# Optimization experiments

Hardware: AMD Instinct MI355X
Metric: run time of the kernel (lower is better)

## Reference

```python
import jax, jax.numpy as jnp
import numpy as np

EPS = 1e-5

def _offset_conv(x, w, b):
    # 3x3 conv, padding=1, producing 2*K*K offset channels (standard DeformConv2D v1)
    out = jax.lax.conv_general_dilated(x, w, (1, 1), ((1, 1), (1, 1)),
                                       dimension_numbers=('NCHW', 'OIHW', 'NCHW'))
    return out + b[None, :, None, None]

def _bilinear_gather(x, py, px):
    # x: [B,C,H,W]; py,px: [B,K2,H,W] float sample coords -> [B,C,K2,H,W]
    B, C, H, W = x.shape
    py = jnp.clip(py, 0.0, H - 1.0)
    px = jnp.clip(px, 0.0, W - 1.0)
    y0 = jnp.floor(py)
    x0 = jnp.floor(px)
    wy = py - y0
    wx = px - x0
    y0i = y0.astype(jnp.int32)
    x0i = x0.astype(jnp.int32)
    y1i = jnp.minimum(y0i + 1, H - 1)
    x1i = jnp.minimum(x0i + 1, W - 1)
    xf = x.reshape(B, C, H * W)
    K2, Ho, Wo = py.shape[1], py.shape[2], py.shape[3]
    def gather(yy, xx):
        idx = (yy * W + xx).reshape(B, 1, -1)  # broadcast over C
        return jnp.take_along_axis(xf, idx, axis=2).reshape(B, C, K2, Ho, Wo)
    v00 = gather(y0i, x0i)
    v01 = gather(y0i, x1i)
    v10 = gather(y1i, x0i)
    v11 = gather(y1i, x1i)
    wy = wy[:, None]
    wx = wx[:, None]
    return (v00 * (1 - wy) * (1 - wx) + v01 * (1 - wy) * wx
            + v10 * wy * (1 - wx) + v11 * wy * wx)

def _deform_dw(x, w_off, b_off, w_dw, k):
    # depthwise deformable conv, kernel k, padding k//2 (same spatial size)
    B, C, H, W = x.shape
    K2 = k * k
    off = _offset_conv(x, w_off, b_off)      # [B, 2*K2, H, W]
    dy, dx = off[:, :K2], off[:, K2:]
    r = (k - 1) // 2
    pn = jnp.arange(-r, r + 1, dtype=x.dtype)
    pn_y = jnp.repeat(pn, k)[None, :, None, None]  # [1,K2,1,1]
    pn_x = jnp.tile(pn, k)[None, :, None, None]
    gy = jnp.arange(H, dtype=x.dtype)[None, None, :, None]
    gx = jnp.arange(W, dtype=x.dtype)[None, None, None, :]
    py = gy + pn_y + dy
    px = gx + pn_x + dx
    samp = _bilinear_gather(x, py, px)        # [B,C,K2,H,W]
    return jnp.einsum('bckhw,ck->bchw', samp, w_dw.reshape(C, K2))

def _bn_relu(x, g, b, m, v):
    inv = g / jnp.sqrt(v + EPS)
    return jax.nn.relu(x * inv[None, :, None, None] + (b - m * inv)[None, :, None, None])

def setup_inputs() -> dict:
    key = jax.random.key(0)
    B, C, H, W, O = 4, 96, 64, 64, 192
    ks = jax.random.split(key, 32)
    d = {'x': jax.random.normal(ks[0], (B, C, H, W), jnp.float32)}
    i = 1
    for k in (3, 5, 7):
        K2 = k * k
        d[f'w_off{k}'] = 0.01 * jax.random.normal(ks[i], (2 * K2, C, 3, 3), jnp.float32); i += 1
        d[f'b_off{k}'] = jnp.zeros((2 * K2,), jnp.float32)
        d[f'w_dw{k}'] = jax.random.normal(ks[i], (C, k, k), jnp.float32) / k; i += 1
        d[f'g{k}'] = jnp.ones((C,), jnp.float32)
        d[f'be{k}'] = jnp.zeros((C,), jnp.float32)
        d[f'm{k}'] = 0.1 * jax.random.normal(ks[i], (C,), jnp.float32); i += 1
        d[f'v{k}'] = jax.random.uniform(ks[i], (C,), jnp.float32, 0.5, 1.5); i += 1
    d['w_pw'] = jax.random.normal(ks[i], (O, 3 * C), jnp.float32) / np.sqrt(3 * C).astype(np.float32); i += 1
    d['gp'] = jnp.ones((O,), jnp.float32)
    d['bp'] = jnp.zeros((O,), jnp.float32)
    d['mp'] = 0.1 * jax.random.normal(ks[i], (O,), jnp.float32); i += 1
    d['vp'] = jax.random.uniform(ks[i], (O,), jnp.float32, 0.5, 1.5)
    return d

def reference(x, w_off3, b_off3, w_dw3, g3, be3, m3, v3,
              w_off5, b_off5, w_dw5, g5, be5, m5, v5,
              w_off7, b_off7, w_dw7, g7, be7, m7, v7,
              w_pw, gp, bp, mp, vp):
    x1 = _bn_relu(_deform_dw(x, w_off3, b_off3, w_dw3, 3), g3, be3, m3, v3)
    x2 = _bn_relu(_deform_dw(x, w_off5, b_off5, w_dw5, 5), g5, be5, m5, v5)
    x3 = _bn_relu(_deform_dw(x, w_off7, b_off7, w_dw7, 7), g7, be7, m7, v7)
    xc = jnp.concatenate([x1, x2, x3], axis=1)  # [B, 3C, H, W]
    out = jnp.einsum('bchw,oc->bohw', xc, w_pw)  # 1x1 conv
    return _bn_relu(out, gp, bp, mp, vp)
```

## Files before the change

### kernel.cpp

```cpp
#include <hip/hip_runtime.h>
#include <math.h>

typedef unsigned short u16;
typedef short s16x8 __attribute__((ext_vector_type(8)));
typedef float f32x4 __attribute__((ext_vector_type(4)));

#define HWp 4096
#define Cc 96
#define Bb 4
#define Oo 192
#define C3 288

#define OFF_OFF   0
#define OFF_WDWT  3145728
#define OFF_BCAT  3159840
#define OFF_SBR   3160032
#define OFF_HBR   3160320
#define OFF_SPW   3160608
#define OFF_HPW   3160800
#define FP32_END  3160992
#define BF_XTPAD  0
#define BF_WOF    1672704
#define BF_WPW    1838592
#define BF_YT     1893888

__device__ __forceinline__ u16 f2bf(float f) {
    union { float f; unsigned u; } t; t.f = f;
    unsigned u = t.u;
    return (u16)((u + 0x7fffu + ((u >> 16) & 1u)) >> 16);
}
__device__ __forceinline__ float bflo(unsigned u) { return __uint_as_float(u << 16); }
__device__ __forceinline__ float bfhi(unsigned u) { return __uint_as_float(u & 0xffff0000u); }

__global__ __launch_bounds__(256) void prep_kernel(
    const float* __restrict__ w3, const float* __restrict__ b3, const float* __restrict__ dw3,
    const float* __restrict__ g3, const float* __restrict__ be3, const float* __restrict__ m3, const float* __restrict__ v3,
    const float* __restrict__ w5, const float* __restrict__ b5, const float* __restrict__ dw5,
    const float* __restrict__ g5, const float* __restrict__ be5, const float* __restrict__ m5, const float* __restrict__ v5,
    const float* __restrict__ w7, const float* __restrict__ b7, const float* __restrict__ dw7,
    const float* __restrict__ g7, const float* __restrict__ be7, const float* __restrict__ m7, const float* __restrict__ v7,
    const float* __restrict__ wpw,
    const float* __restrict__ gp, const float* __restrict__ bp, const float* __restrict__ mp, const float* __restrict__ vp,
    float* __restrict__ ws)
{
    u16* bf = (u16*)(ws + FP32_END);
    int i = blockIdx.x * 256 + threadIdx.x;
    if (i < 165888) {
        int f = i / 13824, r = i % 13824;
        int s = r >> 9, l = r & 511;
        int lane = l >> 3, j = l & 7;
        int o = f * 16 + (lane & 15);
        int k = s * 32 + (lane >> 4) * 8 + j;
        int tap = k / 96, c = k % 96;
        float v = 0.f;
        if (o < 18)       v = w3[o * 864 + c * 9 + tap];
        else if (o < 68)  v = w5[(o - 18) * 864 + c * 9 + tap];
        else if (o < 166) v = w7[(o - 68) * 864 + c * 9 + tap];
        bf[BF_WOF + i] = f2bf(v);
        return;
    }
    int j = i - 165888;
    if (j < 55296) {
        int f = j / 4608, r = j % 4608;
        int s = r >> 9, l = r & 511;
        int lane = l >> 3, jj = l & 7;
        int o = f * 16 + (lane & 15);
        int k = s * 32 + (lane >> 4) * 8 + jj;
        bf[BF_WPW + j] = f2bf(wpw[o * C3 + k]);
        return;
    }
    j -= 55296;
    if (j < 14112) {
        int ksel = j / 4704, rem = j % 4704;
        int t = rem / 96, c = rem % 96;
        int K2 = (ksel == 0) ? 9 : (ksel == 1) ? 25 : 49;
        const float* dw = (ksel == 0) ? dw3 : (ksel == 1) ? dw5 : dw7;
        ws[OFF_WDWT + j] = (t < K2) ? dw[c * K2 + t] : 0.f;
        return;
    }
    j -= 14112;
    if (j < 192) {
        float v = 0.f;
        if (j < 18)       v = b3[j];
        else if (j < 68)  v = b5[j - 18];
        else if (j < 166) v = b7[j - 68];
        ws[OFF_BCAT + j] = v;
        return;
    }
    j -= 192;
    if (j < C3) {
        int ks = j / Cc, c = j % Cc;
        const float* g = (ks == 0) ? g3 : (ks == 1) ? g5 : g7;
        const float* v = (ks == 0) ? v3 : (ks == 1) ? v5 : v7;
        ws[OFF_SBR + j] = g[c] / sqrtf(v[c] + 1e-5f);
        return;
    }
    j -= C3;
    if (j < C3) {
        int ks = j / Cc, c = j % Cc;
        const float* g = (ks == 0) ? g3 : (ks == 1) ? g5 : g7;
        const float* v = (ks == 0) ? v3 : (ks == 1) ? v5 : v7;
        const float* be = (ks == 0) ? be3 : (ks == 1) ? be5 : be7;
        const float* m = (ks == 0) ? m3 : (ks == 1) ? m5 : m7;
        float inv = g[c] / sqrtf(v[c] + 1e-5f);
        ws[OFF_HBR + j] = be[c] - m[c] * inv;
        return;
    }
    j -= C3;
    if (j < Oo) { ws[OFF_SPW + j] = gp[j] / sqrtf(vp[j] + 1e-5f); return; }
    j -= Oo;
    if (j < Oo) {
        float inv = gp[j] / sqrtf(vp[j] + 1e-5f);
        ws[OFF_HPW + j] = bp[j] - mp[j] * inv;
        return;
    }
    j -= Oo;
    if (j < 24960) {
        int c4 = j % 24, rem = j / 24;
        int cell = rem % 260, bb = rem / 260;
        int row, col;
        if (cell < 66)       { row = 0;  col = cell; }
        else if (cell < 132) { row = 65; col = cell - 66; }
        else if (cell < 196) { row = cell - 132 + 1; col = 0; }
        else                 { row = cell - 196 + 1; col = 65; }
        u16* dst = bf + BF_XTPAD + ((size_t)(bb * 66 + row) * 66 + col) * 96 + c4 * 4;
        *(uint2*)dst = make_uint2(0u, 0u);
        return;
    }
}
#define PREP_N (165888 + 55296 + 14112 + 192 + 288 + 288 + 192 + 192 + 24960)

__global__ __launch_bounds__(256) void xtpad_kernel(
    const float* __restrict__ x, float* __restrict__ ws)
{
    __shared__ u16 sT[64 * 104];
    u16* bfm = (u16*)(ws + FP32_END);
    const int tid = threadIdx.x;
    const int h = blockIdx.x, b = blockIdx.y;
    const float* xb = x + (((size_t)b * Cc) << 12) + (h << 6);
#pragma unroll
    for (int it = 0; it < 24; ++it) {
        int j = tid + it * 256;
        int c = j >> 6, p = j & 63;
        sT[p * 104 + c] = f2bf(xb[((size_t)c << 12) + p]);
    }
    __syncthreads();
    u16* dst = bfm + BF_XTPAD + ((size_t)(b * 66 + h + 1) * 66 + 1) * 96;
#pragma unroll
    for (int it = 0; it < 6; ++it) {
        int j = tid + it * 256;
        int pos = j / 24, c4 = j % 24;
        const u16* s = &sT[pos * 104 + c4 * 4];
        *(uint2*)(dst + pos * 96 + c4 * 4) = make_uint2(
            (unsigned)s[0] | ((unsigned)s[1] << 16),
            (unsigned)s[2] | ((unsigned)s[3] << 16));
    }
}

__global__ __launch_bounds__(512) void offconv_mfma(
    const float* __restrict__ ws, float* __restrict__ off)
{
    __shared__ u16 sX[3 * 66 * 98];
    const u16* bf = (const u16*)(ws + FP32_END);
    const u16* xp = bf + BF_XTPAD;
    const u16* wof = bf + BF_WOF;
    const int tid = threadIdx.x;
    const int lane = tid & 63, wid = tid >> 6;
    const int lane15 = lane & 15, quad = lane >> 4;
    const int h = blockIdx.x;
    const int b = blockIdx.z;
    const int f0 = (wid >> 2) * 6;
    const int pos = (wid & 3) * 16 + lane15;

#pragma unroll
    for (int it = 0; it < 10; ++it) {
        int j = tid + it * 512;
        if (j < 4752) {
            int r = j / (66 * 24);
            int rem = j % (66 * 24);
            int col = rem / 24, c4 = rem % 24;
            uint2 v = *(const uint2*)(xp + ((size_t)((b * 66 + h + r) * 66 + col)) * 96 + c4 * 4);
            *(uint2*)(&sX[(r * 66 + col) * 98 + c4 * 4]) = v;
        }
    }
    __syncthreads();

    f32x4 acc[6];
#pragma unroll
    for (int f = 0; f < 6; ++f) acc[f] = (f32x4){0.f, 0.f, 0.f, 0.f};

#pragma unroll
    for (int tap = 0; tap < 9; ++tap) {
        const int ky = tap / 3, kx = tap % 3;
        const u16* brow = &sX[(ky * 66 + kx + pos) * 98 + quad * 8];
#pragma unroll
        for (int cc = 0; cc < 3; ++cc) {
            s16x8 bb = *(const s16x8*)(brow + cc * 32);
            const int s = tap * 3 + cc;
#pragma unroll
            for (int f = 0; f < 6; ++f) {
                s16x8 a = *(const s16x8*)(wof + ((size_t)((f0 + f) * 27 + s) * 64 + lane) * 8);
                acc[f] = __builtin_amdgcn_mfma_f32_16x16x32_bf16(a, bb, acc[f], 0, 0, 0);
            }
        }
    }

    const float* bcat = ws + OFF_BCAT;
    const int p = (h << 6) + pos;
#pragma unroll
    for (int f = 0; f < 6; ++f) {
        float* dst = off + (((size_t)(b * 192 + (f0 + f) * 16 + quad * 4)) << 12) + p;
#pragma unroll
        for (int r = 0; r < 4; ++r)
            dst[(size_t)r << 12] = acc[f][r] + bcat[(f0 + f) * 16 + quad * 4 + r];
    }
}

template<int K>
__device__ __forceinline__ void samp_v6(
    int ksel, float* __restrict__ sWI,
    const float* __restrict__ ws, u16* __restrict__ yt)
{
    constexpr int K2 = K * K;
    constexpr int R = (K - 1) / 2;
    const int tb = (ksel == 0) ? 0 : ((ksel == 1) ? 18 : 68);

    const int tid = threadIdx.x;
    const int b = blockIdx.z;
    const int p0 = blockIdx.x * 20;

    const float* offb = ws + OFF_OFF + ((size_t)(b * 192 + tb)) * HWp;
    for (int i = tid; i < K2 * 20; i += 256) {
        int t = i / 20, q = i % 20;
        int p = min(p0 + q, 4095);
        int hh = p >> 6, wp = p & 63;
        float dy = offb[(size_t)t * HWp + p];
        float dx = offb[(size_t)(K2 + t) * HWp + p];
        int ky = t / K - R, kx = t % K - R;
        float py = fminf(fmaxf((float)(hh + ky) + dy, 0.f), 63.f);
        float px = fminf(fmaxf((float)(wp + kx) + dx, 0.f), 63.f);
        float fy = floorf(py), fx = floorf(px);
        int y0 = (int)fy, x0 = (int)fx;
        float wy = py - fy, wx = px - fx;
        int y1 = min(y0 + 1, 63), x1 = min(x0 + 1, 63);
        float w11 = wy * wx;
        float w10 = wy - w11;
        float w01 = wx - w11;
        float w00 = 1.f - wy - wx + w11;
        float* dst = &sWI[i * 8];
        dst[0] = w00; dst[1] = w01; dst[2] = w10; dst[3] = w11;
        dst[4] = __int_as_float(((y0 + 1) * 66 + x0 + 1) * 96);
        dst[5] = __int_as_float(((y0 + 1) * 66 + x1 + 1) * 96);
        dst[6] = __int_as_float(((y1 + 1) * 66 + x0 + 1) * 96);
        dst[7] = __int_as_float(((y1 + 1) * 66 + x1 + 1) * 96);
    }
    __syncthreads();

    const int c8 = tid % 12;
    const int q  = tid / 12;
    const int p  = p0 + q;
    if (tid < 240 && p < 4096) {
        const int c = c8 * 8;

        const u16* xc = (const u16*)(ws + FP32_END) + BF_XTPAD + (size_t)b * 66 * 66 * 96 + c;
        const float* wdT = ws + OFF_WDWT + ksel * 4704 + c;

        float acc[8];
#pragma unroll
        for (int k = 0; k < 8; ++k) acc[k] = 0.f;

        for (int t = 0; t < K2; ++t) {
            const float4 W = *(const float4*)(&sWI[(t * 20 + q) * 8]);
            const float4 I = *(const float4*)(&sWI[(t * 20 + q) * 8 + 4]);
            const uint4 u00 = *(const uint4*)(xc + __float_as_int(I.x));
            const uint4 u01 = *(const uint4*)(xc + __float_as_int(I.y));
            const uint4 u10 = *(const uint4*)(xc + __float_as_int(I.z));
            const uint4 u11 = *(const uint4*)(xc + __float_as_int(I.w));
            const float4 wda = *(const float4*)(wdT + t * 96);
            const float4 wdb = *(const float4*)(wdT + t * 96 + 4);
            const unsigned a00[4] = {u00.x, u00.y, u00.z, u00.w};
            const unsigned a01[4] = {u01.x, u01.y, u01.z, u01.w};
            const unsigned a10[4] = {u10.x, u10.y, u10.z, u10.w};
            const unsigned a11[4] = {u11.x, u11.y, u11.z, u11.w};
            const float wd[8] = {wda.x, wda.y, wda.z, wda.w, wdb.x, wdb.y, wdb.z, wdb.w};
#pragma unroll
            for (int d = 0; d < 4; ++d) {
                float vlo = fmaf(W.x, bflo(a00[d]), fmaf(W.y, bflo(a01[d]),
                            fmaf(W.z, bflo(a10[d]), W.w * bflo(a11[d]))));
                float vhi = fmaf(W.x, bfhi(a00[d]), fmaf(W.y, bfhi(a01[d]),
                            fmaf(W.z, bfhi(a10[d]), W.w * bfhi(a11[d]))));
                acc[2 * d]     = fmaf(wd[2 * d],     vlo, acc[2 * d]);
                acc[2 * d + 1] = fmaf(wd[2 * d + 1], vhi, acc[2 * d + 1]);
            }
        }

        const int cb = ksel * Cc + c;
        const float4 sa = *(const float4*)(ws + OFF_SBR + cb);
        const float4 sb = *(const float4*)(ws + OFF_SBR + cb + 4);
        const float4 ha = *(const float4*)(ws + OFF_HBR + cb);
        const float4 hb = *(const float4*)(ws + OFF_HBR + cb + 4);
        const float ss[8] = {sa.x, sa.y, sa.z, sa.w, sb.x, sb.y, sb.z, sb.w};
        const float hh8[8] = {ha.x, ha.y, ha.z, ha.w, hb.x, hb.y, hb.z, hb.w};
        unsigned r[4];
#pragma unroll
        for (int d = 0; d < 4; ++d) {
            u16 lo = f2bf(fmaxf(fmaf(acc[2 * d],     ss[2 * d],     hh8[2 * d]),     0.f));
            u16 hi = f2bf(fmaxf(fmaf(acc[2 * d + 1], ss[2 * d + 1], hh8[2 * d + 1]), 0.f));
            r[d] = (unsigned)lo | ((unsigned)hi << 16);
        }
        *(uint4*)(yt + ((size_t)(b << 12) + p) * C3 + cb) = make_uint4(r[0], r[1], r[2], r[3]);
    }
}

__global__ __launch_bounds__(256, 4) void sampdw6_kernel(float* __restrict__ ws)
{
    __shared__ float sWI[49 * 20 * 8];
    u16* yt = (u16*)(ws + FP32_END) + BF_YT;
    const int e = blockIdx.y;
    if (e == 0)      samp_v6<3>(0, sWI, ws, yt);
    else if (e == 1) samp_v6<5>(1, sWI, ws, yt);
    else             samp_v6<7>(2, sWI, ws, yt);
}

__global__ __launch_bounds__(512) void pwconv_mfma(
    const float* __restrict__ ws, float* __restrict__ out)
{
    __shared__ u16 sB[64 * 296];
    const u16* bf = (const u16*)(ws + FP32_END);
    const u16* yt = bf + BF_YT;
    const u16* wpw = bf + BF_WPW;
    const int tid = threadIdx.x;
    const int lane = tid & 63, wid = tid >> 6;
    const int lane15 = lane & 15, quad = lane >> 4;
    const int p0 = blockIdx.x * 64;
    const int b = blockIdx.z;
    const int f0 = (wid >> 2) * 6;
    const int pos = (wid & 3) * 16 + lane15;

#pragma unroll
    for (int it = 0; it < 5; ++it) {
        int j = tid + it * 512;
        if (j < 2304) {
            int ps = j / 36, c8 = j % 36;
            *(uint4*)(&sB[ps * 296 + c8 * 8]) =
                *(const uint4*)(yt + ((size_t)(b << 12) + p0 + ps) * C3 + c8 * 8);
        }
    }
    __syncthreads();

    f32x4 acc[6];
#pragma unroll
    for (int f = 0; f < 6; ++f) acc[f] = (f32x4){0.f, 0.f, 0.f, 0.f};

    const u16* brow = &sB[pos * 296 + quad * 8];
#pragma unroll
    for (int s = 0; s < 9; ++s) {
        s16x8 bb = *(const s16x8*)(brow + s * 32);
#pragma unroll
        for (int f = 0; f < 6; ++f) {
            s16x8 a = *(const s16x8*)(wpw + ((size_t)((f0 + f) * 9 + s) * 64 + lane) * 8);
            acc[f] = __builtin_amdgcn_mfma_f32_16x16x32_bf16(a, bb, acc[f], 0, 0, 0);
        }
    }

    const float* spw = ws + OFF_SPW;
    const float* hpw = ws + OFF_HPW;
    const int p = p0 + pos;
#pragma unroll
    for (int f = 0; f < 6; ++f) {
        float* dst = out + (((size_t)(b * Oo + (f0 + f) * 16 + quad * 4)) << 12) + p;
#pragma unroll
        for (int r = 0; r < 4; ++r) {
            int o = (f0 + f) * 16 + quad * 4 + r;
            dst[(size_t)r << 12] = fmaxf(fmaf(acc[f][r], spw[o], hpw[o]), 0.f);
        }
    }
}

extern "C" void kernel_launch(void* const* d_in, const int* in_sizes, int n_in,
                              void* d_out, int out_size, void* d_ws, size_t ws_size,
                              hipStream_t stream)
{
    const float* x     = (const float*)d_in[0];
    const float* w3    = (const float*)d_in[1];
    const float* b3    = (const float*)d_in[2];
    const float* dw3   = (const float*)d_in[3];
    const float* g3    = (const float*)d_in[4];
    const float* be3   = (const float*)d_in[5];
    const float* m3    = (const float*)d_in[6];
    const float* v3    = (const float*)d_in[7];
    const float* w5    = (const float*)d_in[8];
    const float* b5    = (const float*)d_in[9];
    const float* dw5   = (const float*)d_in[10];
    const float* g5    = (const float*)d_in[11];
    const float* be5   = (const float*)d_in[12];
    const float* m5    = (const float*)d_in[13];
    const float* v5    = (const float*)d_in[14];
    const float* w7    = (const float*)d_in[15];
    const float* b7    = (const float*)d_in[16];
    const float* dw7   = (const float*)d_in[17];
    const float* g7    = (const float*)d_in[18];
    const float* be7   = (const float*)d_in[19];
    const float* m7    = (const float*)d_in[20];
    const float* v7    = (const float*)d_in[21];
    const float* wpw   = (const float*)d_in[22];
    const float* gp    = (const float*)d_in[23];
    const float* bp    = (const float*)d_in[24];
    const float* mp    = (const float*)d_in[25];
    const float* vp    = (const float*)d_in[26];

    float* ws = (float*)d_ws;
    float* out = (float*)d_out;

    {
        prep_kernel<<<(PREP_N + 255) / 256, 256, 0, stream>>>(
            w3, b3, dw3, g3, be3, m3, v3,
            w5, b5, dw5, g5, be5, m5, v5,
            w7, b7, dw7, g7, be7, m7, v7,
            wpw, gp, bp, mp, vp, ws);
    }
    {
        dim3 grid(64, Bb);
        xtpad_kernel<<<grid, 256, 0, stream>>>(x, ws);
    }
    {
        dim3 grid(64, 1, Bb);
        offconv_mfma<<<grid, 512, 0, stream>>>(ws, ws + OFF_OFF);
    }
    {
        dim3 grid(205, 3, Bb);
        sampdw6_kernel<<<grid, 256, 0, stream>>>(ws);
    }
    {
        dim3 grid(64, 1, Bb);
        pwconv_mfma<<<grid, 512, 0, stream>>>(ws, out);
    }
}
```

Before: 208.9 us.

## Switch to fp16 storage with packed half2 bilinear math, fuse transpose into prep, rebalance sampling

Replaces bf16 with fp16 for the padded input, weights and intermediate activations, using f16 MFMA and packed half2 FMAs for the bilinear interpolation. The sample-info table in shared memory is compressed to one uint4 per tap, holding half2 weights plus a base offset and packed deltas. The x transpose/pad kernel is merged into the prep kernel, removing one launch. The sampling grid is reorganised so 3x3 and 5x5 blocks process several 20-pixel rounds, balancing work across kernel sizes, and occupancy is raised to 6 blocks. Doing the interpolation in fp16 risks some accuracy loss, and values outside the fp16 range could overflow.

```diff
diff --git a/kernel.cpp b/kernel.cpp
--- a/kernel.cpp
+++ b/kernel.cpp
@@ -1,8 +1,9 @@
 #include <hip/hip_runtime.h>
+#include <hip/hip_fp16.h>
 #include <math.h>
 
 typedef unsigned short u16;
-typedef short s16x8 __attribute__((ext_vector_type(8)));
+typedef _Float16 f16x8 __attribute__((ext_vector_type(8)));
 typedef float f32x4 __attribute__((ext_vector_type(4)));
 
 #define HWp 4096
@@ -24,15 +25,15 @@
 #define BF_WPW    1838592
 #define BF_YT     1893888
 
-__device__ __forceinline__ u16 f2bf(float f) {
-    union { float f; unsigned u; } t; t.f = f;
-    unsigned u = t.u;
-    return (u16)((u + 0x7fffu + ((u >> 16) & 1u)) >> 16);
-}
-__device__ __forceinline__ float bflo(unsigned u) { return __uint_as_float(u << 16); }
-__device__ __forceinline__ float bfhi(unsigned u) { return __uint_as_float(u & 0xffff0000u); }
+__device__ __forceinline__ u16 f2h(float f) { return __half_as_ushort(__float2half(f)); }
+__device__ __forceinline__ unsigned h2u(__half2 h) { union { __half2 h; unsigned u; } t; t.h = h; return t.u; }
+__device__ __forceinline__ __half2 u2h(unsigned u) { union { __half2 h; unsigned u; } t; t.u = u; return t.h; }
+
+#define PREP_N (165888 + 55296 + 14112 + 192 + 288 + 288 + 192 + 192 + 24960)
+#define PREP_BLK ((PREP_N + 255) / 256)
 
 __global__ __launch_bounds__(256) void prep_kernel(
+    const float* __restrict__ x,
     const float* __restrict__ w3, const float* __restrict__ b3, const float* __restrict__ dw3,
     const float* __restrict__ g3, const float* __restrict__ be3, const float* __restrict__ m3, const float* __restrict__ v3,
     const float* __restrict__ w5, const float* __restrict__ b5, const float* __restrict__ dw5,
@@ -43,8 +44,34 @@
     const float* __restrict__ gp, const float* __restrict__ bp, const float* __restrict__ mp, const float* __restrict__ vp,
     float* __restrict__ ws)
 {
+    __shared__ u16 sT[64 * 104];
     u16* bf = (u16*)(ws + FP32_END);
-    int i = blockIdx.x * 256 + threadIdx.x;
+    const int tid = threadIdx.x;
+
+    if (blockIdx.x < 256) {
+        const int b = blockIdx.x >> 6, h = blockIdx.x & 63;
+        const float* xb = x + (((size_t)b * Cc) << 12) + (h << 6);
+#pragma unroll
+        for (int it = 0; it < 24; ++it) {
+            int j = tid + it * 256;
+            int c = j >> 6, p = j & 63;
+            sT[p * 104 + c] = f2h(xb[((size_t)c << 12) + p]);
+        }
+        __syncthreads();
+        u16* dst = bf + BF_XTPAD + ((size_t)(b * 66 + h + 1) * 66 + 1) * 96;
+#pragma unroll
+        for (int it = 0; it < 6; ++it) {
+            int j = tid + it * 256;
+            int pos = j / 24, c4 = j % 24;
+            const u16* s = &sT[pos * 104 + c4 * 4];
+            *(uint2*)(dst + pos * 96 + c4 * 4) = make_uint2(
+                (unsigned)s[0] | ((unsigned)s[1] << 16),
+                (unsigned)s[2] | ((unsigned)s[3] << 16));
+        }
+        return;
+    }
+
+    int i = (blockIdx.x - 256) * 256 + tid;
     if (i < 165888) {
         int f = i / 13824, r = i % 13824;
         int s = r >> 9, l = r & 511;
@@ -56,7 +83,7 @@
         if (o < 18)       v = w3[o * 864 + c * 9 + tap];
         else if (o < 68)  v = w5[(o - 18) * 864 + c * 9 + tap];
         else if (o < 166) v = w7[(o - 68) * 864 + c * 9 + tap];
-        bf[BF_WOF + i] = f2bf(v);
+        bf[BF_WOF + i] = f2h(v);
         return;
     }
     int j = i - 165888;
@@ -66,7 +93,7 @@
         int lane = l >> 3, jj = l & 7;
         int o = f * 16 + (lane & 15);
         int k = s * 32 + (lane >> 4) * 8 + jj;
-        bf[BF_WPW + j] = f2bf(wpw[o * C3 + k]);
+        bf[BF_WPW + j] = f2h(wpw[o * C3 + k]);
         return;
     }
     j -= 55296;
@@ -128,34 +155,6 @@
         return;
     }
 }
-#define PREP_N (165888 + 55296 + 14112 + 192 + 288 + 288 + 192 + 192 + 24960)
-
-__global__ __launch_bounds__(256) void xtpad_kernel(
-    const float* __restrict__ x, float* __restrict__ ws)
-{
-    __shared__ u16 sT[64 * 104];
-    u16* bfm = (u16*)(ws + FP32_END);
-    const int tid = threadIdx.x;
-    const int h = blockIdx.x, b = blockIdx.y;
-    const float* xb = x + (((size_t)b * Cc) << 12) + (h << 6);
-#pragma unroll
-    for (int it = 0; it < 24; ++it) {
-        int j = tid + it * 256;
-        int c = j >> 6, p = j & 63;
-        sT[p * 104 + c] = f2bf(xb[((size_t)c << 12) + p]);
-    }
-    __syncthreads();
-    u16* dst = bfm + BF_XTPAD + ((size_t)(b * 66 + h + 1) * 66 + 1) * 96;
-#pragma unroll
-    for (int it = 0; it < 6; ++it) {
-        int j = tid + it * 256;
-        int pos = j / 24, c4 = j % 24;
-        const u16* s = &sT[pos * 104 + c4 * 4];
-        *(uint2*)(dst + pos * 96 + c4 * 4) = make_uint2(
-            (unsigned)s[0] | ((unsigned)s[1] << 16),
-            (unsigned)s[2] | ((unsigned)s[3] << 16));
-    }
-}
 
 __global__ __launch_bounds__(512) void offconv_mfma(
     const float* __restrict__ ws, float* __restrict__ off)
@@ -195,12 +194,12 @@
         const u16* brow = &sX[(ky * 66 + kx + pos) * 98 + quad * 8];
 #pragma unroll
         for (int cc = 0; cc < 3; ++cc) {
-            s16x8 bb = *(const s16x8*)(brow + cc * 32);
+            f16x8 bb = *(const f16x8*)(brow + cc * 32);
             const int s = tap * 3 + cc;
 #pragma unroll
             for (int f = 0; f < 6; ++f) {
-                s16x8 a = *(const s16x8*)(wof + ((size_t)((f0 + f) * 27 + s) * 64 + lane) * 8);
-                acc[f] = __builtin_amdgcn_mfma_f32_16x16x32_bf16(a, bb, acc[f], 0, 0, 0);
+                f16x8 a = *(const f16x8*)(wof + ((size_t)((f0 + f) * 27 + s) * 64 + lane) * 8);
+                acc[f] = __builtin_amdgcn_mfma_f32_16x16x32_f16(a, bb, acc[f], 0, 0, 0);
             }
         }
     }
@@ -217,8 +216,8 @@
 }
 
 template<int K>
-__device__ __forceinline__ void samp_v6(
-    int ksel, float* __restrict__ sWI,
+__device__ __forceinline__ void samp_v7(
+    int ksel, int p0, int rounds, uint4* __restrict__ sWI,
     const float* __restrict__ ws, u16* __restrict__ yt)
 {
     constexpr int K2 = K * K;
@@ -227,99 +226,104 @@
 
     const int tid = threadIdx.x;
     const int b = blockIdx.z;
-    const int p0 = blockIdx.x * 20;
-
     const float* offb = ws + OFF_OFF + ((size_t)(b * 192 + tb)) * HWp;
-    for (int i = tid; i < K2 * 20; i += 256) {
-        int t = i / 20, q = i % 20;
-        int p = min(p0 + q, 4095);
-        int hh = p >> 6, wp = p & 63;
-        float dy = offb[(size_t)t * HWp + p];
-        float dx = offb[(size_t)(K2 + t) * HWp + p];
-        int ky = t / K - R, kx = t % K - R;
-        float py = fminf(fmaxf((float)(hh + ky) + dy, 0.f), 63.f);
-        float px = fminf(fmaxf((float)(wp + kx) + dx, 0.f), 63.f);
-        float fy = floorf(py), fx = floorf(px);
-        int y0 = (int)fy, x0 = (int)fx;
-        float wy = py - fy, wx = px - fx;
-        int y1 = min(y0 + 1, 63), x1 = min(x0 + 1, 63);
-        float w11 = wy * wx;
-        float w10 = wy - w11;
-        float w01 = wx - w11;
-        float w00 = 1.f - wy - wx + w11;
-        float* dst = &sWI[i * 8];
-        dst[0] = w00; dst[1] = w01; dst[2] = w10; dst[3] = w11;
-        dst[4] = __int_as_float(((y0 + 1) * 66 + x0 + 1) * 96);
-        dst[5] = __int_as_float(((y0 + 1) * 66 + x1 + 1) * 96);
-        dst[6] = __int_as_float(((y1 + 1) * 66 + x0 + 1) * 96);
-        dst[7] = __int_as_float(((y1 + 1) * 66 + x1 + 1) * 96);
-    }
-    __syncthreads();
-
     const int c8 = tid % 12;
     const int q  = tid / 12;
-    const int p  = p0 + q;
-    if (tid < 240 && p < 4096) {
-        const int c = c8 * 8;
-
-        const u16* xc = (const u16*)(ws + FP32_END) + BF_XTPAD + (size_t)b * 66 * 66 * 96 + c;
-        const float* wdT = ws + OFF_WDWT + ksel * 4704 + c;
-
-        float acc[8];
-#pragma unroll
-        for (int k = 0; k < 8; ++k) acc[k] = 0.f;
-
-        for (int t = 0; t < K2; ++t) {
-            const float4 W = *(const float4*)(&sWI[(t * 20 + q) * 8]);
-            const float4 I = *(const float4*)(&sWI[(t * 20 + q) * 8 + 4]);
-            const uint4 u00 = *(const uint4*)(xc + __float_as_int(I.x));
-            const uint4 u01 = *(const uint4*)(xc + __float_as_int(I.y));
-            const uint4 u10 = *(const uint4*)(xc + __float_as_int(I.z));
-            const uint4 u11 = *(const uint4*)(xc + __float_as_int(I.w));
-            const float4 wda = *(const float4*)(wdT + t * 96);
-            const float4 wdb = *(const float4*)(wdT + t * 96 + 4);
-            const unsigned a00[4] = {u00.x, u00.y, u00.z, u00.w};
-            const unsigned a01[4] = {u01.x, u01.y, u01.z, u01.w};
-            const unsigned a10[4] = {u10.x, u10.y, u10.z, u10.w};
-            const unsigned a11[4] = {u11.x, u11.y, u11.z, u11.w};
-            const float wd[8] = {wda.x, wda.y, wda.z, wda.w, wdb.x, wdb.y, wdb.z, wdb.w};
+    const int c = c8 * 8;
+    const u16* xh = (const u16*)(ws + FP32_END) + BF_XTPAD + (size_t)b * 66 * 66 * 96;
+    const char* xcb = (const char*)xh + c * 2;
+    const float* wdT = ws + OFF_WDWT + ksel * 4704 + c;
+
+    for (int r = 0; r < rounds; ++r) {
+        const int p0r = p0 + r * 20;
+        for (int i = tid; i < K2 * 20; i += 256) {
+            int t = i / 20, qq = i % 20;
+            int p = min(p0r + qq, 4095);
+            int hh = p >> 6, wp = p & 63;
+            float dy = offb[(size_t)t * HWp + p];
+            float dx = offb[(size_t)(K2 + t) * HWp + p];
+            int ky = t / K - R, kx = t % K - R;
+            float py = fminf(fmaxf((float)(hh + ky) + dy, 0.f), 63.f);
+            float px = fminf(fmaxf((float)(wp + kx) + dx, 0.f), 63.f);
+            float fy = floorf(py), fx = floorf(px);
+            int y0 = (int)fy, x0 = (int)fx;
+            float wy = py - fy, wx = px - fx;
+            int y1 = min(y0 + 1, 63), x1 = min(x0 + 1, 63);
+            float w11 = wy * wx;
+            float w10 = wy - w11;
+            float w01 = wx - w11;
+            float w00 = 1.f - wy - wx + w11;
+            unsigned wA = h2u(__floats2half2_rn(w00, w01));
+            unsigned wB = h2u(__floats2half2_rn(w10, w11));
+            unsigned o00 = (unsigned)((y0 + 1) * 66 + (x0 + 1)) * 192u;
+            unsigned d01 = (unsigned)(x1 - x0) * 192u;
+            unsigned d10 = (unsigned)(y1 - y0) * 12672u;
+            sWI[i] = make_uint4(wA, wB, o00, d01 | (d10 << 16));
+        }
+        __syncthreads();
+
+        const int p = p0r + q;
+        if (tid < 240 && p < 4096) {
+            float acc[8];
+#pragma unroll
+            for (int k = 0; k < 8; ++k) acc[k] = 0.f;
+
+            for (int t = 0; t < K2; ++t) {
+                const uint4 e = sWI[t * 20 + q];
+                const __half2 wA = u2h(e.x), wB = u2h(e.y);
+                const __half2 w00b = __low2half2(wA), w01b = __high2half2(wA);
+                const __half2 w10b = __low2half2(wB), w11b = __high2half2(wB);
+                const unsigned d01 = e.w & 0xffffu, d10 = e.w >> 16;
+                const uint4 u00 = *(const uint4*)(xcb + e.z);
+                const uint4 u01 = *(const uint4*)(xcb + e.z + d01);
+                const uint4 u10 = *(const uint4*)(xcb + e.z + d10);
+                const uint4 u11 = *(const uint4*)(xcb + e.z + d10 + d01);
+                const float4 wda = *(const float4*)(wdT + t * 96);
+                const float4 wdb = *(const float4*)(wdT + t * 96 + 4);
+                const unsigned a00[4] = {u00.x, u00.y, u00.z, u00.w};
+                const unsigned a01[4] = {u01.x, u01.y, u01.z, u01.w};
+                const unsigned a10[4] = {u10.x, u10.y, u10.z, u10.w};
+                const unsigned a11[4] = {u11.x, u11.y, u11.z, u11.w};
+                const float wd[8] = {wda.x, wda.y, wda.z, wda.w, wdb.x, wdb.y, wdb.z, wdb.w};
+#pragma unroll
+                for (int d = 0; d < 4; ++d) {
+                    __half2 v = __hmul2(w00b, u2h(a00[d]));
+                    v = __hfma2(w01b, u2h(a01[d]), v);
+                    v = __hfma2(w10b, u2h(a10[d]), v);
+                    v = __hfma2(w11b, u2h(a11[d]), v);
+                    acc[2 * d]     = fmaf(wd[2 * d],     __low2float(v),  acc[2 * d]);
+                    acc[2 * d + 1] = fmaf(wd[2 * d + 1], __high2float(v), acc[2 * d + 1]);
+                }
+            }
+
+            const int cb = ksel * Cc + c;
+            const float4 sa = *(const float4*)(ws + OFF_SBR + cb);
+            const float4 sb = *(const float4*)(ws + OFF_SBR + cb + 4);
+            const float4 ha = *(const float4*)(ws + OFF_HBR + cb);
+            const float4 hb = *(const float4*)(ws + OFF_HBR + cb + 4);
+            const float ss[8] = {sa.x, sa.y, sa.z, sa.w, sb.x, sb.y, sb.z, sb.w};
+            const float hh8[8] = {ha.x, ha.y, ha.z, ha.w, hb.x, hb.y, hb.z, hb.w};
+            unsigned rr[4];
 #pragma unroll
             for (int d = 0; d < 4; ++d) {
-                float vlo = fmaf(W.x, bflo(a00[d]), fmaf(W.y, bflo(a01[d]),
-                            fmaf(W.z, bflo(a10[d]), W.w * bflo(a11[d]))));
-                float vhi = fmaf(W.x, bfhi(a00[d]), fmaf(W.y, bfhi(a01[d]),
-                            fmaf(W.z, bfhi(a10[d]), W.w * bfhi(a11[d]))));
-                acc[2 * d]     = fmaf(wd[2 * d],     vlo, acc[2 * d]);
-                acc[2 * d + 1] = fmaf(wd[2 * d + 1], vhi, acc[2 * d + 1]);
+                float lo = fmaxf(fmaf(acc[2 * d],     ss[2 * d],     hh8[2 * d]),     0.f);
+                float hi = fmaxf(fmaf(acc[2 * d + 1], ss[2 * d + 1], hh8[2 * d + 1]), 0.f);
+                rr[d] = h2u(__floats2half2_rn(lo, hi));
             }
-        }
-
-        const int cb = ksel * Cc + c;
-        const float4 sa = *(const float4*)(ws + OFF_SBR + cb);
-        const float4 sb = *(const float4*)(ws + OFF_SBR + cb + 4);
-        const float4 ha = *(const float4*)(ws + OFF_HBR + cb);
-        const float4 hb = *(const float4*)(ws + OFF_HBR + cb + 4);
-        const float ss[8] = {sa.x, sa.y, sa.z, sa.w, sb.x, sb.y, sb.z, sb.w};
-        const float hh8[8] = {ha.x, ha.y, ha.z, ha.w, hb.x, hb.y, hb.z, hb.w};
-        unsigned r[4];
-#pragma unroll
-        for (int d = 0; d < 4; ++d) {
-            u16 lo = f2bf(fmaxf(fmaf(acc[2 * d],     ss[2 * d],     hh8[2 * d]),     0.f));
-            u16 hi = f2bf(fmaxf(fmaf(acc[2 * d + 1], ss[2 * d + 1], hh8[2 * d + 1]), 0.f));
-            r[d] = (unsigned)lo | ((unsigned)hi << 16);
-        }
-        *(uint4*)(yt + ((size_t)(b << 12) + p) * C3 + cb) = make_uint4(r[0], r[1], r[2], r[3]);
-    }
-}
-
-__global__ __launch_bounds__(256, 4) void sampdw6_kernel(float* __restrict__ ws)
-{
-    __shared__ float sWI[49 * 20 * 8];
+            *(uint4*)(yt + ((size_t)(b << 12) + p) * C3 + cb) = make_uint4(rr[0], rr[1], rr[2], rr[3]);
+        }
+        if (r + 1 < rounds) __syncthreads();
+    }
+}
+
+__global__ __launch_bounds__(256, 6) void sampdw7_kernel(float* __restrict__ ws)
+{
+    __shared__ uint4 sWI[980];
     u16* yt = (u16*)(ws + FP32_END) + BF_YT;
-    const int e = blockIdx.y;
-    if (e == 0)      samp_v6<3>(0, sWI, ws, yt);
-    else if (e == 1) samp_v6<5>(1, sWI, ws, yt);
-    else             samp_v6<7>(2, sWI, ws, yt);
+    const int bx = blockIdx.x;
+    if (bx < 41)        samp_v7<3>(0, bx * 100, 5, sWI, ws, yt);
+    else if (bx < 144)  samp_v7<5>(1, (bx - 41) * 40, 2, sWI, ws, yt);
+    else                samp_v7<7>(2, (bx - 144) * 20, 1, sWI, ws, yt);
 }
 
 __global__ __launch_bounds__(512) void pwconv_mfma(
@@ -355,11 +359,11 @@
     const u16* brow = &sB[pos * 296 + quad * 8];
 #pragma unroll
     for (int s = 0; s < 9; ++s) {
-        s16x8 bb = *(const s16x8*)(brow + s * 32);
+        f16x8 bb = *(const f16x8*)(brow + s * 32);
 #pragma unroll
         for (int f = 0; f < 6; ++f) {
-            s16x8 a = *(const s16x8*)(wpw + ((size_t)((f0 + f) * 9 + s) * 64 + lane) * 8);
-            acc[f] = __builtin_amdgcn_mfma_f32_16x16x32_bf16(a, bb, acc[f], 0, 0, 0);
+            f16x8 a = *(const f16x8*)(wpw + ((size_t)((f0 + f) * 9 + s) * 64 + lane) * 8);
+            acc[f] = __builtin_amdgcn_mfma_f32_16x16x32_f16(a, bb, acc[f], 0, 0, 0);
         }
     }
 
@@ -413,23 +417,20 @@
     float* out = (float*)d_out;
 
     {
-        prep_kernel<<<(PREP_N + 255) / 256, 256, 0, stream>>>(
+        prep_kernel<<<256 + PREP_BLK, 256, 0, stream>>>(
+            x,
             w3, b3, dw3, g3, be3, m3, v3,
             w5, b5, dw5, g5, be5, m5, v5,
             w7, b7, dw7, g7, be7, m7, v7,
             wpw, gp, bp, mp, vp, ws);
     }
     {
-        dim3 grid(64, Bb);
-        xtpad_kernel<<<grid, 256, 0, stream>>>(x, ws);
-    }
-    {
         dim3 grid(64, 1, Bb);
         offconv_mfma<<<grid, 512, 0, stream>>>(ws, ws + OFF_OFF);
     }
     {
-        dim3 grid(205, 3, Bb);
-        sampdw6_kernel<<<grid, 256, 0, stream>>>(ws);
+        dim3 grid(349, 1, Bb);
+        sampdw7_kernel<<<grid, 256, 0, stream>>>(ws);
     }
     {
         dim3 grid(64, 1, Bb);
```

Measured after the change: 191.0 us. 8.6% less time.
